# Performance work log

Hardware: AMD Instinct MI355X
Metric: run time of the kernel (lower is better)

## Reference

```python
import jax, jax.numpy as jnp
import numpy as np

N, H, W, DIM = 8, 32, 32, 768
HEAD_DIM = 64
NUM_HEADS = DIM // HEAD_DIM
KERNEL = (7, 7)
ROT_DIM = HEAD_DIM // 2  # 32
POS_DIM = 2
THETA = 10000.0
LN_EPS = 1e-5


def setup_inputs() -> dict:
    key = jax.random.key(0)
    k_x, k_qkv, k_out = jax.random.split(key, 3)
    S = H * W
    x = jax.random.normal(k_x, (N, S, DIM), dtype=jnp.float32)
    # 2D grid positions, same for every batch element
    grid = jnp.stack(jnp.meshgrid(jnp.arange(H), jnp.arange(W), indexing='ij'), axis=-1)
    pos = jnp.broadcast_to(grid.reshape(1, S, 2), (N, S, 2)).astype(jnp.int32)
    padding_mask = jnp.ones((N, S), dtype=bool)
    ln_g = jnp.ones((DIM,), dtype=jnp.float32)
    ln_b = jnp.zeros((DIM,), dtype=jnp.float32)
    w_qkv = jax.random.normal(k_qkv, (DIM, 3 * DIM), dtype=jnp.float32) * 0.02
    b_qkv = jnp.zeros((3 * DIM,), dtype=jnp.float32)
    w_out = jax.random.normal(k_out, (DIM, DIM), dtype=jnp.float32) * 0.02
    b_out = jnp.zeros((DIM,), dtype=jnp.float32)
    return {"x": x, "pos": pos, "padding_mask": padding_mask,
            "ln_g": ln_g, "ln_b": ln_b,
            "w_qkv": w_qkv, "b_qkv": b_qkv,
            "w_out": w_out, "b_out": b_out}


def _rope_cos_sin(pos):
    # freqs: theta ** linspace(0, -1, rot_dim // (pos_dim*2) + 1)[:-1] -> 8 freqs
    n_freq = ROT_DIM // (POS_DIM * 2)
    freqs = THETA ** jnp.linspace(0.0, -1.0, n_freq + 1, dtype=jnp.float32)[:-1]
    # pos: [n, s, 2] -> [n, s, 2, n_freq] -> [n, s, 2*n_freq] -> [n, 1, s, 2*n_freq]
    tmp = (pos[..., None].astype(jnp.float32) * freqs).reshape(*pos.shape[:-1], -1)[:, None]
    return jnp.cos(tmp), jnp.sin(tmp)


def _apply_rotary(x, cos, sin):
    d = cos.shape[-1]  # 16
    x1, x2, x3 = x[..., :d], x[..., d:2 * d], x[..., 2 * d:]
    y1 = x1 * cos - x2 * sin
    y2 = x2 * cos + x1 * sin
    return jnp.concatenate((y1.astype(x3.dtype), y2.astype(x3.dtype), x3), axis=-1)


def _attn_mask(pos, padding_mask, kernel_size):
    dh = pos[:, :, None, 0] - pos[:, None, :, 0]  # [n, s, s]
    dw = pos[:, :, None, 1] - pos[:, None, :, 1]
    kh, kw = kernel_size
    m = ((dh <= kh // 2) & (dh > -((kh + 1) // 2))
         & (dw <= kw // 2) & (dw > -((kw + 1) // 2)))
    m = m & (padding_mask[:, None, :] & padding_mask[:, :, None])
    return m[:, None]  # [n, 1, s, s]


def reference(x, pos, padding_mask, ln_g, ln_b, w_qkv, b_qkv, w_out, b_out):
    n, s, dim = x.shape
    skip = x
    # LayerNorm
    mu = jnp.mean(x, axis=-1, keepdims=True)
    var = jnp.mean(jnp.square(x - mu), axis=-1, keepdims=True)
    xn = (x - mu) * jax.lax.rsqrt(var + LN_EPS) * ln_g + ln_b
    # QKV projection; split 'n s (t h d)'
    qkv = xn @ w_qkv + b_qkv                       # [n, s, 3*dim]
    qkv = qkv.reshape(n, s, 3, NUM_HEADS, HEAD_DIM)
    qkv = jnp.transpose(qkv, (2, 0, 3, 1, 4))      # [3, n, h, s, d]
    q, k, v = qkv[0], qkv[1], qkv[2]
    # RoPE on first half of head dim
    cos, sin = _rope_cos_sin(pos)
    q = _apply_rotary(q, cos, sin)
    k = _apply_rotary(k, cos, sin)
    # Local 2D-window masked SDPA
    mask = _attn_mask(pos, padding_mask, KERNEL)   # [n, 1, s, s]
    scale = 1.0 / jnp.sqrt(jnp.asarray(HEAD_DIM, dtype=q.dtype))
    scores = jnp.einsum('nhqd,nhkd->nhqk', q, k) * scale
    scores = jnp.where(mask, scores, jnp.asarray(-1e30, dtype=scores.dtype))
    attn = jax.nn.softmax(scores, axis=-1)
    o = jnp.einsum('nhqk,nhkd->nhqd', attn, v)     # [n, h, s, d]
    o = jnp.transpose(o, (0, 2, 1, 3)).reshape(n, s, dim)
    return o @ w_out + b_out + skip
```

## Files before the change

### kernel.cpp

```cpp
#include <hip/hip_runtime.h>


typedef unsigned short u16;
typedef unsigned int   u32;
typedef __attribute__((ext_vector_type(8))) short v8s;
typedef __attribute__((ext_vector_type(4))) float v4f;
typedef __attribute__((ext_vector_type(4))) unsigned short v4us;

#define MFMA16(a,b,c) __builtin_amdgcn_mfma_f32_16x16x32_bf16((a),(b),(c),0,0,0)

__device__ __forceinline__ u16 f2bf(float f){
  union { float f; u32 u; } v; v.f = f;
  u32 u = v.u;
  u32 r = u + 0x7FFFu + ((u >> 16) & 1u);
  return (u16)(r >> 16);
}
__device__ __forceinline__ float bf2f(u16 h){
  union { u32 u; float f; } v; v.u = ((u32)h) << 16;
  return v.f;
}
__device__ __forceinline__ void gll16(const void* g, void* l){
  __builtin_amdgcn_global_load_lds((const __attribute__((address_space(1))) void*)g,
                                   (__attribute__((address_space(3))) void*)l, 16, 0, 0);
}
__device__ __forceinline__ v8s ld8(const u16* p){ return *(const v8s*)p; }
__device__ __forceinline__ void st8(u16* p, v8s v){ *(v8s*)p = v; }

__global__ __launch_bounds__(256) void jet_transpose(const float* __restrict__ in,
                                                     u16* __restrict__ out, int R, int C){
  __shared__ float tile[32][33];
  const int bx = blockIdx.x << 5, by = blockIdx.y << 5;
  const int tx = threadIdx.x & 31, ty = threadIdx.x >> 5;
  #pragma unroll
  for (int i = 0; i < 32; i += 8)
    tile[ty + i][tx] = in[(size_t)(by + ty + i) * C + bx + tx];
  __syncthreads();
  #pragma unroll
  for (int i = 0; i < 32; i += 8)
    out[(size_t)(bx + ty + i) * R + by + tx] = f2bf(tile[tx][ty + i]);
}

__global__ __launch_bounds__(256) void jet_ln(const float* __restrict__ x,
                                              const float* __restrict__ g,
                                              const float* __restrict__ b,
                                              u16* __restrict__ xn){
  const int row = blockIdx.x;
  const int t = threadIdx.x;
  const float* xr = x + (size_t)row * 768;
  float a0 = xr[t], a1 = xr[t + 256], a2 = xr[t + 512];
  float s  = a0 + a1 + a2;
  float ss = a0*a0 + a1*a1 + a2*a2;
  #pragma unroll
  for (int o = 1; o < 64; o <<= 1){ s += __shfl_xor(s, o); ss += __shfl_xor(ss, o); }
  __shared__ float red[8];
  const int wv = t >> 6, lane = t & 63;
  if (lane == 0){ red[wv] = s; red[4 + wv] = ss; }
  __syncthreads();
  s  = red[0] + red[1] + red[2] + red[3];
  ss = red[4] + red[5] + red[6] + red[7];
  const float mu = s * (1.0f / 768.0f);
  const float var = ss * (1.0f / 768.0f) - mu * mu;
  const float rs = rsqrtf(var + 1e-5f);
  u16* o = xn + (size_t)row * 768;
  o[t]       = f2bf((a0 - mu) * rs * g[t]       + b[t]);
  o[t + 256] = f2bf((a1 - mu) * rs * g[t + 256] + b[t + 256]);
  o[t + 512] = f2bf((a2 - mu) * rs * g[t + 512] + b[t + 512]);
}

template<int MODE>
__global__ __launch_bounds__(256, 4)
void jet_gemm(const u16* __restrict__ A, const u16* __restrict__ Bt,
              const float* __restrict__ bias, int K,
              u16* __restrict__ qbuf, u16* __restrict__ kbuf, u16* __restrict__ vbuf,
              const float* __restrict__ skip, float* __restrict__ outp)
{
  __shared__ u16 As[2][128 * 32];
  __shared__ u16 Bs[2][128 * 32];
  const int tid = threadIdx.x;
  const int lane = tid & 63, wv = tid >> 6;
  const int wm = wv >> 1, wn = wv & 1;
  const int row0 = blockIdx.x * 128, col0 = blockIdx.y * 128;
  const int lq = lane & 15, lk = lane >> 4;

  v4f acc[4][4] = {};

  auto stage = [&](int bsel, int kt){
    const int k0 = kt * 32;
    #pragma unroll
    for (int i = 0; i < 2; ++i){
      const int lin = i * 256 + tid;
      const int r = lin >> 2, c = lin & 3;
      const int sc = c ^ ((r >> 1) & 3);
      gll16(A  + (size_t)(row0 + r) * K + k0 + (sc << 3), (void*)&As[bsel][lin << 3]);
      gll16(Bt + (size_t)(col0 + r) * K + k0 + (sc << 3), (void*)&Bs[bsel][lin << 3]);
    }
  };

  stage(0, 0);
  __syncthreads();
  const int KT = K >> 5;
  for (int kt = 0; kt < KT; ++kt){
    const int cur = kt & 1;
    if (kt + 1 < KT) stage(cur ^ 1, kt + 1);
    v8s af[4], bf[4];
    #pragma unroll
    for (int m = 0; m < 4; ++m){
      const int row_ = wm*64 + m*16 + lq;
      af[m] = ld8(&As[cur][row_*32 + ((lk ^ ((row_ >> 1) & 3)) << 3)]);
    }
    #pragma unroll
    for (int n = 0; n < 4; ++n){
      const int row_ = wn*64 + n*16 + lq;
      bf[n] = ld8(&Bs[cur][row_*32 + ((lk ^ ((row_ >> 1) & 3)) << 3)]);
    }
    #pragma unroll
    for (int m = 0; m < 4; ++m)
      #pragma unroll
      for (int n = 0; n < 4; ++n)
        acc[m][n] = MFMA16(af[m], bf[n], acc[m][n]);
    __syncthreads();
  }

  if (MODE == 0){
    const int colw = col0 + wn * 64;
    const int which = colw / 768;
    const int cm = colw - which * 768;
    const int hh = cm >> 6;
    float bb[4];
    #pragma unroll
    for (int n = 0; n < 4; ++n) bb[n] = bias[colw + n * 16 + lq];

    if (which == 2){
      #pragma unroll
      for (int m = 0; m < 4; ++m){
        const int rbase = row0 + wm * 64 + m * 16 + lk * 4;
        const int img = rbase >> 10, s = rbase & 1023;
        u16* vp = vbuf + (size_t)(img * 12 + hh) * 64 * 1024;
        #pragma unroll
        for (int n = 0; n < 4; ++n){
          const int d = n * 16 + lq;
          v4us pk;
          #pragma unroll
          for (int r = 0; r < 4; ++r) pk[r] = f2bf(acc[m][n][r] + bb[n]);
          *(v4us*)&vp[(size_t)d * 1024 + s] = pk;
        }
      }
    } else {
      u16* dst0 = (which == 0) ? qbuf : kbuf;
      const float freq = __expf(-(float)(lq & 7) * 1.1512925464970229f);
      #pragma unroll
      for (int m = 0; m < 4; ++m){
        const int rbase = row0 + wm * 64 + m * 16 + lk * 4;
        const int img = rbase >> 10, sb = rbase & 1023;
        u16* dst = dst0 + ((size_t)(img * 12 + hh) * 1024 + sb) * 64;
        #pragma unroll
        for (int r = 0; r < 4; ++r){
          const int s = sb + r;
          const float coord = (float)((lq < 8) ? (s >> 5) : (s & 31));
          float sn, cs;
          __sincosf(coord * freq, &sn, &cs);
          const float x1 = acc[m][0][r] + bb[0];
          const float x2 = acc[m][1][r] + bb[1];
          u16* dr = dst + (size_t)r * 64;
          dr[lq]      = f2bf(x1 * cs - x2 * sn);
          dr[16 + lq] = f2bf(x2 * cs + x1 * sn);
          dr[32 + lq] = f2bf(acc[m][2][r] + bb[2]);
          dr[48 + lq] = f2bf(acc[m][3][r] + bb[3]);
        }
      }
    }
  } else {
    #pragma unroll
    for (int m = 0; m < 4; ++m){
      const int rbase = row0 + wm*64 + m*16 + lk*4;
      #pragma unroll
      for (int n = 0; n < 4; ++n){
        const int col = col0 + wn*64 + n*16 + lq;
        const float bb = bias[col];
        const size_t o = (size_t)rbase * 768 + col;
        #pragma unroll
        for (int r = 0; r < 4; ++r)
          outp[o + (size_t)r * 768] = acc[m][n][r] + bb + skip[o + (size_t)r * 768];
      }
    }
  }
}

__global__ __launch_bounds__(256, 4)
void jet_attn(const u16* __restrict__ qbuf, const u16* __restrict__ kbuf,
              const u16* __restrict__ vbuf, u16* __restrict__ obuf)
{
  __shared__ u16  Ps[32][232];
  __shared__ float red_m[2][2][16];
  __shared__ float red_s[2][2][16];
  __shared__ u16  Os[32][72];

  const int blk0 = blockIdx.x;
  const int blk = (blk0 & 7) * 384 + (blk0 >> 3);
  const int qh = blk & 31;
  const int nh = blk >> 5;
  const int img = nh / 12, hd = nh - img * 12;
  int h0 = qh - 3; h0 = h0 < 0 ? 0 : (h0 > 25 ? 25 : h0);
  const int s0q = qh * 32, s0k = h0 * 32;
  const int tid = threadIdx.x;
  const int lane = tid & 63, wv = tid >> 6;
  const int lq = lane & 15, lk = lane >> 4;
  const int qg = wv & 1, kh = wv >> 1;

  const u16* kg = kbuf + ((size_t)nh * 1024 + s0k) * 64;
  const u16* vg = vbuf + (size_t)nh * 64 * 1024;

  const u16* qrow = qbuf + ((size_t)nh * 1024 + s0q + qg * 16 + lq) * 64;
  const v8s qf0 = ld8(qrow + lk * 8);
  const v8s qf1 = ld8(qrow + 32 + lk * 8);

  float sc[28];
  const int qw = qg * 16 + lq;
  #pragma unroll
  for (int t = 0; t < 7; ++t){
    const int tile = kh * 7 + t;
    const u16* krow = kg + (size_t)(tile * 16 + lq) * 64;
    const v8s kf0 = ld8(krow + lk * 8);
    const v8s kf1 = ld8(krow + 32 + lk * 8);
    v4f s = {0.f, 0.f, 0.f, 0.f};
    s = MFMA16(kf0, qf0, s);
    s = MFMA16(kf1, qf1, s);
    #pragma unroll
    for (int r = 0; r < 4; ++r){
      const int k = tile * 16 + lk * 4 + r;
      const int dh = qh - (h0 + (k >> 5));
      const int dw = qw - (k & 31);
      const bool ok = (dh <= 3) & (dh >= -3) & (dw <= 3) & (dw >= -3);
      sc[t * 4 + r] = ok ? s[r] * 0.125f : -1e30f;
    }
  }

  float mx = -1e30f;
  #pragma unroll
  for (int i = 0; i < 28; ++i) mx = fmaxf(mx, sc[i]);
  mx = fmaxf(mx, __shfl_xor(mx, 16));
  mx = fmaxf(mx, __shfl_xor(mx, 32));
  if (lk == 0) red_m[qg][kh][lq] = mx;
  __syncthreads();
  const float m_all = fmaxf(mx, red_m[qg][kh ^ 1][lq]);

  float sum = 0.f;
  #pragma unroll
  for (int i = 0; i < 28; ++i){
    const float e = __expf(sc[i] - m_all);
    sc[i] = e; sum += e;
  }
  #pragma unroll
  for (int t = 0; t < 7; ++t){
    v4us pk;
    #pragma unroll
    for (int r = 0; r < 4; ++r) pk[r] = f2bf(sc[t * 4 + r]);
    *(v4us*)&Ps[qw][kh * 112 + t * 16 + lk * 4] = pk;
  }
  sum += __shfl_xor(sum, 16);
  sum += __shfl_xor(sum, 32);
  if (lk == 0) red_s[qg][kh][lq] = sum;
  __syncthreads();

  const int qg2 = wv & 1, dh2 = wv >> 1;
  v4f acc0 = {0.f, 0.f, 0.f, 0.f}, acc1 = {0.f, 0.f, 0.f, 0.f};
  #pragma unroll
  for (int ks = 0; ks < 7; ++ks){
    const v8s af = ld8(&Ps[qg2 * 16 + lq][ks * 32 + lk * 8]);
    const v8s b0 = ld8(vg + (size_t)(dh2 * 32 + lq) * 1024 + s0k + ks * 32 + lk * 8);
    const v8s b1 = ld8(vg + (size_t)(dh2 * 32 + 16 + lq) * 1024 + s0k + ks * 32 + lk * 8);
    acc0 = MFMA16(af, b0, acc0);
    acc1 = MFMA16(af, b1, acc1);
  }
  {
    const int qi = lk * 4;
    #pragma unroll
    for (int r = 0; r < 4; ++r){
      const float inv = 1.0f / (red_s[qg2][0][qi + r] + red_s[qg2][1][qi + r]);
      Os[qg2 * 16 + qi + r][dh2 * 32 + lq]      = f2bf(acc0[r] * inv);
      Os[qg2 * 16 + qi + r][dh2 * 32 + 16 + lq] = f2bf(acc1[r] * inv);
    }
  }
  __syncthreads();
  {
    const int r = tid >> 3, c = (tid & 7) * 8;
    u16* dst = obuf + ((size_t)img * 1024 + s0q + r) * 768 + hd * 64 + c;
    st8(dst, ld8(&Os[r][c]));
  }
}

extern "C" void kernel_launch(void* const* d_in, const int* in_sizes, int n_in,
                              void* d_out, int out_size, void* d_ws, size_t ws_size,
                              hipStream_t stream)
{
  const float* x     = (const float*)d_in[0];
  const float* ln_g  = (const float*)d_in[3];
  const float* ln_b  = (const float*)d_in[4];
  const float* w_qkv = (const float*)d_in[5];
  const float* b_qkv = (const float*)d_in[6];
  const float* w_out = (const float*)d_in[7];
  const float* b_out = (const float*)d_in[8];
  float* out = (float*)d_out;

  char* ws = (char*)d_ws;
  size_t off = 0;
  auto alloc = [&](size_t n){ size_t o = off; off += (n + 255) & ~(size_t)255; return o; };
  u16* xn    = (u16*)(ws + alloc(8192ull * 768 * 2));
  u16* wqkvT = (u16*)(ws + alloc(2304ull * 768 * 2));
  u16* woutT = (u16*)(ws + alloc(768ull  * 768 * 2));
  u16* q_buf = (u16*)(ws + alloc(96ull * 1024 * 64 * 2));
  u16* k_buf = (u16*)(ws + alloc(96ull * 1024 * 64 * 2));
  u16* v_buf = (u16*)(ws + alloc(96ull * 1024 * 64 * 2));
  u16* o_buf = (u16*)(ws + alloc(8192ull * 768 * 2));

  jet_transpose<<<dim3(2304 / 32, 768 / 32), 256, 0, stream>>>(w_qkv, wqkvT, 768, 2304);
  jet_transpose<<<dim3(768 / 32, 768 / 32),  256, 0, stream>>>(w_out, woutT, 768, 768);
  jet_ln<<<8192, 256, 0, stream>>>(x, ln_g, ln_b, xn);
  jet_gemm<0><<<dim3(64, 18), 256, 0, stream>>>(xn, wqkvT, b_qkv, 768,
                                                q_buf, k_buf, v_buf, nullptr, nullptr);
  jet_attn<<<8 * 12 * 32, 256, 0, stream>>>(q_buf, k_buf, v_buf, o_buf);
  jet_gemm<1><<<dim3(64, 6), 256, 0, stream>>>(o_buf, woutT, b_out, 768,
                                               nullptr, nullptr, nullptr, x, out);
}
```

Baseline: 135.5 us.

## Merge prep kernels and load GEMM operands directly from global memory

The two weight transposes and the LayerNorm are merged into one launch, which saves two kernel launches. The GEMM drops its LDS double-buffering and barriers. Each wave now loads MFMA fragments straight from global memory into registers, with register double-buffering and a fixed K. The GEMM grid becomes 1-D with a block-index swizzle for L2 locality, and the occupancy hint moves from 4 to 3. The risk is that global loads are no longer shared between waves through LDS, so cache traffic rises, and each lane reads only 16 bytes per row, which coalesces poorly.

```diff
diff --git a/kernel.cpp b/kernel.cpp
--- a/kernel.cpp
+++ b/kernel.cpp
@@ -19,106 +19,106 @@
   union { u32 u; float f; } v; v.u = ((u32)h) << 16;
   return v.f;
 }
-__device__ __forceinline__ void gll16(const void* g, void* l){
-  __builtin_amdgcn_global_load_lds((const __attribute__((address_space(1))) void*)g,
-                                   (__attribute__((address_space(3))) void*)l, 16, 0, 0);
-}
 __device__ __forceinline__ v8s ld8(const u16* p){ return *(const v8s*)p; }
 __device__ __forceinline__ void st8(u16* p, v8s v){ *(v8s*)p = v; }
 
-__global__ __launch_bounds__(256) void jet_transpose(const float* __restrict__ in,
-                                                     u16* __restrict__ out, int R, int C){
-  __shared__ float tile[32][33];
-  const int bx = blockIdx.x << 5, by = blockIdx.y << 5;
-  const int tx = threadIdx.x & 31, ty = threadIdx.x >> 5;
-  #pragma unroll
-  for (int i = 0; i < 32; i += 8)
-    tile[ty + i][tx] = in[(size_t)(by + ty + i) * C + bx + tx];
-  __syncthreads();
-  #pragma unroll
-  for (int i = 0; i < 32; i += 8)
-    out[(size_t)(bx + ty + i) * R + by + tx] = f2bf(tile[tx][ty + i]);
-}
-
-__global__ __launch_bounds__(256) void jet_ln(const float* __restrict__ x,
-                                              const float* __restrict__ g,
-                                              const float* __restrict__ b,
-                                              u16* __restrict__ xn){
-  const int row = blockIdx.x;
-  const int t = threadIdx.x;
-  const float* xr = x + (size_t)row * 768;
-  float a0 = xr[t], a1 = xr[t + 256], a2 = xr[t + 512];
-  float s  = a0 + a1 + a2;
-  float ss = a0*a0 + a1*a1 + a2*a2;
-  #pragma unroll
-  for (int o = 1; o < 64; o <<= 1){ s += __shfl_xor(s, o); ss += __shfl_xor(ss, o); }
-  __shared__ float red[8];
-  const int wv = t >> 6, lane = t & 63;
-  if (lane == 0){ red[wv] = s; red[4 + wv] = ss; }
-  __syncthreads();
-  s  = red[0] + red[1] + red[2] + red[3];
-  ss = red[4] + red[5] + red[6] + red[7];
-  const float mu = s * (1.0f / 768.0f);
-  const float var = ss * (1.0f / 768.0f) - mu * mu;
-  const float rs = rsqrtf(var + 1e-5f);
-  u16* o = xn + (size_t)row * 768;
-  o[t]       = f2bf((a0 - mu) * rs * g[t]       + b[t]);
-  o[t + 256] = f2bf((a1 - mu) * rs * g[t + 256] + b[t + 256]);
-  o[t + 512] = f2bf((a2 - mu) * rs * g[t + 512] + b[t + 512]);
+__global__ __launch_bounds__(256)
+void jet_prep(const float* __restrict__ x, const float* __restrict__ g,
+              const float* __restrict__ b, u16* __restrict__ xn,
+              const float* __restrict__ w0, u16* __restrict__ t0,
+              const float* __restrict__ w1, u16* __restrict__ t1)
+{
+  __shared__ float sh[32 * 33];
+  const int bid = blockIdx.x, t = threadIdx.x;
+  if (bid < 8192){
+    const float* xr = x + (size_t)bid * 768;
+    float a0 = xr[t], a1 = xr[t + 256], a2 = xr[t + 512];
+    float s  = a0 + a1 + a2;
+    float ss = a0*a0 + a1*a1 + a2*a2;
+    #pragma unroll
+    for (int o = 1; o < 64; o <<= 1){ s += __shfl_xor(s, o); ss += __shfl_xor(ss, o); }
+    const int wv = t >> 6, lane = t & 63;
+    if (lane == 0){ sh[wv] = s; sh[4 + wv] = ss; }
+    __syncthreads();
+    s  = sh[0] + sh[1] + sh[2] + sh[3];
+    ss = sh[4] + sh[5] + sh[6] + sh[7];
+    const float mu = s * (1.0f / 768.0f);
+    const float var = ss * (1.0f / 768.0f) - mu * mu;
+    const float rs = rsqrtf(var + 1e-5f);
+    u16* o = xn + (size_t)bid * 768;
+    o[t]       = f2bf((a0 - mu) * rs * g[t]       + b[t]);
+    o[t + 256] = f2bf((a1 - mu) * rs * g[t + 256] + b[t + 256]);
+    o[t + 512] = f2bf((a2 - mu) * rs * g[t + 512] + b[t + 512]);
+  } else {
+    const float* in; u16* out; int C, bx, by;
+    if (bid < 8192 + 1728){
+      const int tb = bid - 8192; in = w0; out = t0; C = 2304; bx = tb % 72; by = tb / 72;
+    } else {
+      const int tb = bid - 8192 - 1728; in = w1; out = t1; C = 768; bx = tb % 24; by = tb / 24;
+    }
+    float (*tile)[33] = (float(*)[33])sh;
+    const int x0 = bx << 5, y0 = by << 5;
+    const int tx = t & 31, ty = t >> 5;
+    #pragma unroll
+    for (int i = 0; i < 32; i += 8)
+      tile[ty + i][tx] = in[(size_t)(y0 + ty + i) * C + x0 + tx];
+    __syncthreads();
+    #pragma unroll
+    for (int i = 0; i < 32; i += 8)
+      out[(size_t)(x0 + ty + i) * 768 + y0 + tx] = f2bf(tile[tx][ty + i]);
+  }
 }
 
 template<int MODE>
-__global__ __launch_bounds__(256, 4)
-void jet_gemm(const u16* __restrict__ A, const u16* __restrict__ Bt,
-              const float* __restrict__ bias, int K,
-              u16* __restrict__ qbuf, u16* __restrict__ kbuf, u16* __restrict__ vbuf,
-              const float* __restrict__ skip, float* __restrict__ outp)
+__global__ __launch_bounds__(256, 3)
+void jet_gemm_direct(const u16* __restrict__ A, const u16* __restrict__ Bt,
+                     const float* __restrict__ bias,
+                     u16* __restrict__ qbuf, u16* __restrict__ kbuf, u16* __restrict__ vbuf,
+                     const float* __restrict__ skip, float* __restrict__ outp)
 {
-  __shared__ u16 As[2][128 * 32];
-  __shared__ u16 Bs[2][128 * 32];
+  constexpr int K = 768;
+  constexpr int NB = (MODE == 0) ? 18 : 6;
   const int tid = threadIdx.x;
   const int lane = tid & 63, wv = tid >> 6;
   const int wm = wv >> 1, wn = wv & 1;
-  const int row0 = blockIdx.x * 128, col0 = blockIdx.y * 128;
   const int lq = lane & 15, lk = lane >> 4;
 
+  const int bid = blockIdx.x;
+  const int swz = (bid & 7) * (8 * NB) + (bid >> 3);
+  const int bm = swz / NB, bn = swz - bm * NB;
+  const int row0 = bm * 128, col0 = bn * 128;
+
+  const u16* pa[4]; const u16* pb[4];
+  #pragma unroll
+  for (int m = 0; m < 4; ++m) pa[m] = A + (size_t)(row0 + wm*64 + m*16 + lq) * K + lk*8;
+  #pragma unroll
+  for (int n = 0; n < 4; ++n) pb[n] = Bt + (size_t)(col0 + wn*64 + n*16 + lq) * K + lk*8;
+
   v4f acc[4][4] = {};
-
-  auto stage = [&](int bsel, int kt){
-    const int k0 = kt * 32;
-    #pragma unroll
-    for (int i = 0; i < 2; ++i){
-      const int lin = i * 256 + tid;
-      const int r = lin >> 2, c = lin & 3;
-      const int sc = c ^ ((r >> 1) & 3);
-      gll16(A  + (size_t)(row0 + r) * K + k0 + (sc << 3), (void*)&As[bsel][lin << 3]);
-      gll16(Bt + (size_t)(col0 + r) * K + k0 + (sc << 3), (void*)&Bs[bsel][lin << 3]);
-    }
-  };
-
-  stage(0, 0);
-  __syncthreads();
-  const int KT = K >> 5;
-  for (int kt = 0; kt < KT; ++kt){
-    const int cur = kt & 1;
-    if (kt + 1 < KT) stage(cur ^ 1, kt + 1);
-    v8s af[4], bf[4];
-    #pragma unroll
-    for (int m = 0; m < 4; ++m){
-      const int row_ = wm*64 + m*16 + lq;
-      af[m] = ld8(&As[cur][row_*32 + ((lk ^ ((row_ >> 1) & 3)) << 3)]);
-    }
-    #pragma unroll
-    for (int n = 0; n < 4; ++n){
-      const int row_ = wn*64 + n*16 + lq;
-      bf[n] = ld8(&Bs[cur][row_*32 + ((lk ^ ((row_ >> 1) & 3)) << 3)]);
-    }
+  v8s a0[4], b0[4], a1[4], b1[4];
+  #pragma unroll
+  for (int i = 0; i < 4; ++i){ a0[i] = ld8(pa[i]); b0[i] = ld8(pb[i]); }
+
+  #pragma unroll 1
+  for (int kt = 0; kt < 24; kt += 2){
+    #pragma unroll
+    for (int i = 0; i < 4; ++i){ a1[i] = ld8(pa[i] + 32); b1[i] = ld8(pb[i] + 32); }
     #pragma unroll
     for (int m = 0; m < 4; ++m)
       #pragma unroll
       for (int n = 0; n < 4; ++n)
-        acc[m][n] = MFMA16(af[m], bf[n], acc[m][n]);
-    __syncthreads();
+        acc[m][n] = MFMA16(a0[m], b0[n], acc[m][n]);
+    if (kt + 2 < 24){
+      #pragma unroll
+      for (int i = 0; i < 4; ++i){ a0[i] = ld8(pa[i] + 64); b0[i] = ld8(pb[i] + 64); }
+    }
+    #pragma unroll
+    for (int m = 0; m < 4; ++m)
+      #pragma unroll
+      for (int n = 0; n < 4; ++n)
+        acc[m][n] = MFMA16(a1[m], b1[n], acc[m][n]);
+    #pragma unroll
+    for (int i = 0; i < 4; ++i){ pa[i] += 64; pb[i] += 64; }
   }
 
   if (MODE == 0){
@@ -313,12 +313,10 @@
   u16* v_buf = (u16*)(ws + alloc(96ull * 1024 * 64 * 2));
   u16* o_buf = (u16*)(ws + alloc(8192ull * 768 * 2));
 
-  jet_transpose<<<dim3(2304 / 32, 768 / 32), 256, 0, stream>>>(w_qkv, wqkvT, 768, 2304);
-  jet_transpose<<<dim3(768 / 32, 768 / 32),  256, 0, stream>>>(w_out, woutT, 768, 768);
-  jet_ln<<<8192, 256, 0, stream>>>(x, ln_g, ln_b, xn);
-  jet_gemm<0><<<dim3(64, 18), 256, 0, stream>>>(xn, wqkvT, b_qkv, 768,
-                                                q_buf, k_buf, v_buf, nullptr, nullptr);
+  jet_prep<<<8192 + 1728 + 576, 256, 0, stream>>>(x, ln_g, ln_b, xn, w_qkv, wqkvT, w_out, woutT);
+  jet_gemm_direct<0><<<64 * 18, 256, 0, stream>>>(xn, wqkvT, b_qkv,
+                                                  q_buf, k_buf, v_buf, nullptr, nullptr);
   jet_attn<<<8 * 12 * 32, 256, 0, stream>>>(q_buf, k_buf, v_buf, o_buf);
-  jet_gemm<1><<<dim3(64, 6), 256, 0, stream>>>(o_buf, woutT, b_out, 768,
-                                               nullptr, nullptr, nullptr, x, out);
-}
+  jet_gemm_direct<1><<<64 * 6, 256, 0, stream>>>(o_buf, woutT, b_out,
+                                                 nullptr, nullptr, nullptr, x, out);
+}
```

Result: slower. 221.8 us (+63.7%).
